# Optimization experiments

Hardware: AMD Instinct MI355X
Metric: run time of the kernel (lower is better)

## Reference

```python
import jax, jax.numpy as jnp
import numpy as np

C = 128   # recurrent/value channels
CK = 64   # key channels

def conv1x1(x, W, b):
    # x: [B,Cin,H,W], W: [Cout,Cin], b: [Cout]
    return jnp.einsum('bchw,oc->bohw', x, W) + b[None, :, None, None]

def extract_windows(x):
    # zero-padded 3x3 windows, matching F.unfold(kernel=3, padding=1)
    # x: [B,C,H2,W2] -> [B,C,9,H2,W2], tap order = (ky, kx) row-major
    B, c, H2, W2 = x.shape
    xp = jnp.pad(x, ((0, 0), (0, 0), (1, 1), (1, 1)))
    taps = [xp[:, :, dy:dy + H2, dx:dx + W2] for dy in range(3) for dx in range(3)]
    return jnp.stack(taps, axis=2)

def setup_inputs() -> dict:
    key = jax.random.key(0)
    ks = jax.random.split(key, 12)
    B, H, W = 2, 256, 512
    H2, W2 = 128, 256
    s = 0.02
    return {
        'h_prev': jax.random.normal(ks[0], (B, C, H2, W2), jnp.float32),
        'h_init': jax.random.normal(ks[1], (B, C, H, W), jnp.float32),
        'Wq':   jax.random.normal(ks[2], (CK, C), jnp.float32) * s,
        'bq':   jnp.zeros((CK,), jnp.float32),
        'Wk':   jax.random.normal(ks[3], (CK, C), jnp.float32) * s,
        'bk':   jnp.zeros((CK,), jnp.float32),
        'Wvp':  jax.random.normal(ks[4], (C, C), jnp.float32) * s,
        'bvp':  jnp.zeros((C,), jnp.float32),
        'Wvi':  jax.random.normal(ks[5], (C, C), jnp.float32) * s,
        'bvi':  jnp.zeros((C,), jnp.float32),
        'Wout': jax.random.normal(ks[6], (C, C), jnp.float32) * s,
        'bout': jnp.zeros((C,), jnp.float32),
    }

def reference(h_prev, h_init, Wq, bq, Wk, bk, Wvp, bvp, Wvi, bvi, Wout, bout):
    B, _, H, W = h_init.shape
    _, _, H2, W2 = h_prev.shape
    ry, rx = H // H2, W // W2

    q = conv1x1(h_init, Wq, bq)        # [B,CK,H,W]
    k = conv1x1(h_prev, Wk, bk)        # [B,CK,H2,W2]
    v = conv1x1(h_prev, Wvp, bvp)      # [B,C,H2,W2]

    k_win = extract_windows(k)         # [B,CK,9,H2,W2]
    v_win = extract_windows(v)         # [B,C,9,H2,W2]

    # q at fine res, grouped by coarse cell (nearest-neighbor broadcast of k/v)
    q_r = q.transpose(0, 2, 3, 1).reshape(B, H2, ry, W2, rx, CK)  # [B,H2,ry,W2,rx,CK]
    # scores over 9 window taps (zero-padded taps give score 0, as in unfold)
    scores = jnp.einsum('byaxdc,bcjyx->byaxdj', q_r, k_win)       # [B,H2,ry,W2,rx,9]
    a = jax.nn.softmax(scores, axis=-1)
    x = jnp.einsum('byaxdj,bcjyx->bcyaxd', a, v_win)              # [B,C,H2,ry,W2,rx]
    x = x.reshape(B, C, H, W)

    v_init = conv1x1(h_init, Wvi, bvi)
    return conv1x1(v_init + x, Wout, bout)
```

## Files before the change

kernel.cpp:

```cpp
#include <hip/hip_runtime.h>
#include <cstdint>
#include <cstddef>

#define THREADS 256
#define FTHREADS 512

typedef __attribute__((ext_vector_type(8))) short short8;
typedef __attribute__((ext_vector_type(4))) float f32x4;

#define MFMA(a, b, c) __builtin_amdgcn_mfma_f32_16x16x32_bf16((a), (b), (c), 0, 0, 0)

static constexpr int kC    = 128;
static constexpr int kImgC = 128 * 256;
static constexpr int kImgF = 256 * 512;

__device__ __forceinline__ unsigned short f2bf(float f) {
  unsigned u = __builtin_bit_cast(unsigned, f);
  u += 0x7fffu + ((u >> 16) & 1u);
  return (unsigned short)(u >> 16);
}
__device__ __forceinline__ unsigned pack_bf16(float lo, float hi) {
  return (unsigned)f2bf(lo) | ((unsigned)f2bf(hi) << 16);
}
__device__ __forceinline__ float bf_up(unsigned short u) {
  return __builtin_bit_cast(float, (unsigned)u << 16);
}
__device__ __forceinline__ float bf_lo(unsigned u) {
  return __builtin_bit_cast(float, u << 16);
}
__device__ __forceinline__ float bf_hi(unsigned u) {
  return __builtin_bit_cast(float, u & 0xffff0000u);
}

__device__ __forceinline__ short8 ldA(const char* lds, int mt, int kt, int l) {
  const int px = mt * 16 + (l & 15);
  const int chunk = (kt * 4 + (l >> 4)) ^ (px & 7);
  return *(const short8*)(lds + px * 256 + chunk * 16);
}

__global__ __launch_bounds__(THREADS) void cast_w(
    const float* __restrict__ Wq, const float* __restrict__ Wk,
    const float* __restrict__ Wvp, const float* __restrict__ Wvi,
    const float* __restrict__ Wout, unsigned short* __restrict__ dst) {
  int i = blockIdx.x * THREADS + threadIdx.x;
  float v;
  if (i < 8192)       v = Wq[i];
  else if (i < 16384) v = Wk[i - 8192];
  else if (i < 32768) v = Wvp[i - 16384];
  else if (i < 49152) v = Wvi[i - 32768];
  else                v = Wout[i - 49152];
  dst[i] = f2bf(v);
}

__global__ __launch_bounds__(THREADS, 4) void coarse_kv(
    const float* __restrict__ h_prev, const unsigned short* __restrict__ wbuf,
    const float* __restrict__ bk, const float* __restrict__ bvp,
    unsigned short* __restrict__ kbuf, unsigned short* __restrict__ vbuf) {
  __shared__ char xs[16384];
  const int tid = threadIdx.x;
  const int l = tid & 63, w = tid >> 6;
  const int m = l & 15, g = l >> 4;
  const int chq = w * 16 + m;

  const int tile = blockIdx.x;
  const int b    = tile >> 9;
  const int p0   = (tile & 511) * 64;
  const int p0g  = tile * 64;

  const short8* wkp = (const short8*)(wbuf + 8192);
  const short8* wvp = (const short8*)(wbuf + 16384);
  short8 fk[4], fv[2][4];
  #pragma unroll
  for (int kt = 0; kt < 4; ++kt) fk[kt] = wkp[chq * 16 + kt * 4 + g];
  #pragma unroll
  for (int nt = 0; nt < 2; ++nt)
    #pragma unroll
    for (int kt = 0; kt < 4; ++kt)
      fv[nt][kt] = wvp[(nt * 64 + chq) * 16 + kt * 4 + g];

  {
    const float* src = h_prev + (size_t)b * kC * kImgC + p0;
    const int pxl = l & 7, cg = l >> 3;
    #pragma unroll
    for (int i = 0; i < 16; ++i) {
      const int px = pxl + 8 * (i & 7);
      const int c  = 2 * (cg + 8 * (w + 4 * (i >> 3)));
      float f0 = src[(size_t)c * kImgC + px];
      float f1 = src[(size_t)(c + 1) * kImgC + px];
      const int chunk = (c >> 3) ^ (px & 7);
      *(unsigned*)(xs + px * 256 + chunk * 16 + (c & 7) * 2) = pack_bf16(f0, f1);
    }
  }
  __syncthreads();

  {
    const float bl = bk[chq];
    #pragma unroll
    for (int mt = 0; mt < 4; ++mt) {
      f32x4 acc = {bl, bl, bl, bl};
      #pragma unroll
      for (int kt = 0; kt < 4; ++kt) acc = MFMA(ldA(xs, mt, kt, l), fk[kt], acc);
      #pragma unroll
      for (int r = 0; r < 4; ++r)
        kbuf[(size_t)(p0g + mt * 16 + g * 4 + r) * 64 + chq] = f2bf(acc[r]);
    }
  }
  #pragma unroll
  for (int nt = 0; nt < 2; ++nt) {
    const float bl = bvp[nt * 64 + chq];
    #pragma unroll
    for (int mt = 0; mt < 4; ++mt) {
      f32x4 acc = {bl, bl, bl, bl};
      #pragma unroll
      for (int kt = 0; kt < 4; ++kt) acc = MFMA(ldA(xs, mt, kt, l), fv[nt][kt], acc);
      #pragma unroll
      for (int r = 0; r < 4; ++r)
        vbuf[(size_t)(p0g + mt * 16 + g * 4 + r) * 128 + nt * 64 + chq] = f2bf(acc[r]);
    }
  }
}

__global__ __launch_bounds__(FTHREADS, 4) void fine_fused(
    const float* __restrict__ h_init, const unsigned short* __restrict__ wbuf,
    const float* __restrict__ bq, const float* __restrict__ bvi,
    const float* __restrict__ bout,
    const unsigned short* __restrict__ kbuf, const unsigned short* __restrict__ vbuf,
    float* __restrict__ out) {
  __shared__ char xs[32768];
  __shared__ unsigned short qs[128 * 72];
  __shared__ unsigned short ks_[60 * 80];
  __shared__ unsigned short vs_[60 * 144];

  const int tid = threadIdx.x;
  const int l = tid & 63, w = tid >> 6;
  const int m = l & 15, g = l >> 4;

  const int bid = blockIdx.x;
  const int b   = bid >> 10;
  const int r10 = bid & 1023;
  const int ty  = r10 >> 5;
  const int tx  = r10 & 31;
  const int y0  = ty * 8;
  const int x0  = tx * 16;
  const int y20 = y0 >> 1;
  const int x20 = x0 >> 1;

  const size_t fbase = (size_t)b * kC * kImgF;
  const unsigned short* kb = kbuf + (size_t)b * kImgC * 64;
  const unsigned short* vb = vbuf + (size_t)b * kImgC * 128;

  const short8* wqp = (const short8*)wbuf;
  const short8* wip = (const short8*)(wbuf + 32768);
  const short8* wop = (const short8*)(wbuf + 49152);

  {
    const int half = tid >> 8;
    const int tl = tid & 255;
    const int sl = tl & 63, sw = tl >> 6;
    const int pxl = sl & 7, cg = sl >> 3;
    #pragma unroll
    for (int i = 0; i < 16; ++i) {
      const int px = half * 64 + pxl + 8 * (i & 7);
      const int row = px >> 4, col = px & 15;
      const int c  = 2 * (cg + 8 * (sw + 4 * (i >> 3)));
      const size_t off = (size_t)(y0 + row) * 512 + x0 + col;
      float f0 = h_init[fbase + (size_t)c * kImgF + off];
      float f1 = h_init[fbase + (size_t)(c + 1) * kImgF + off];
      const int chunk = (c >> 3) ^ (px & 7);
      *(unsigned*)(xs + px * 256 + chunk * 16 + (c & 7) * 2) = pack_bf16(f0, f1);
    }
  }

  #pragma unroll
  for (int it = 0; it < 2; ++it) {
    const int i = tid + it * 512;
    if (i < 960) {
      const int cell = i >> 4, cp = i & 15;
      const int cy = cell / 10, cx = cell - cy * 10;
      const int yy = y20 + cy - 1, xx = x20 + cx - 1;
      uint2 val = make_uint2(0u, 0u);
      if ((unsigned)yy < 128u && (unsigned)xx < 256u)
        val = *(const uint2*)(kb + ((size_t)yy * 256 + xx) * 64 + cp * 4);
      *(uint2*)((char*)ks_ + cell * 160 + (cp >> 2) * 40 + (cp & 3) * 8) = val;
    }
  }
  #pragma unroll
  for (int it = 0; it < 4; ++it) {
    const int i = tid + it * 512;
    if (i < 1920) {
      const int cell = i >> 5, cp = i & 31;
      const int cy = cell / 10, cx = cell - cy * 10;
      const int yy = y20 + cy - 1, xx = x20 + cx - 1;
      uint2 val = make_uint2(0u, 0u);
      if ((unsigned)yy < 128u && (unsigned)xx < 256u)
        val = *(const uint2*)(vb + ((size_t)yy * 256 + xx) * 128 + cp * 4);
      *(uint2*)((char*)vs_ + cell * 288 + (cp >> 3) * 72 + (cp & 7) * 8) = val;
    }
  }
  __syncthreads();

  const int chq4 = (w & 3) * 16 + m;
  const int hh   = w >> 2;
  {
    short8 fq[4];
    #pragma unroll
    for (int kt = 0; kt < 4; ++kt) fq[kt] = wqp[chq4 * 16 + kt * 4 + g];
    const float bl = bq[chq4];
    #pragma unroll
    for (int mt = 0; mt < 4; ++mt) {
      f32x4 acc = {bl, bl, bl, bl};
      #pragma unroll
      for (int kt = 0; kt < 4; ++kt) acc = MFMA(ldA(xs, hh * 4 + mt, kt, l), fq[kt], acc);
      #pragma unroll
      for (int r = 0; r < 4; ++r)
        qs[(hh * 64 + mt * 16 + g * 4 + r) * 72 + chq4] = f2bf(acc[r]);
    }
  }

  const int ch = w * 16 + m;
  f32x4 vacc[8];
  {
    short8 fi[4];
    #pragma unroll
    for (int kt = 0; kt < 4; ++kt) fi[kt] = wip[ch * 16 + kt * 4 + g];
    const float bl = bvi[ch];
    #pragma unroll
    for (int mt = 0; mt < 8; ++mt) {
      f32x4 acc = {bl, bl, bl, bl};
      #pragma unroll
      for (int kt = 0; kt < 4; ++kt) acc = MFMA(ldA(xs, mt, kt, l), fi[kt], acc);
      vacc[mt] = acc;
    }
  }
  __syncthreads();

  #pragma unroll
  for (int mt = 0; mt < 8; ++mt) {
    #pragma unroll
    for (int r = 0; r < 4; ++r) {
      const int px = mt * 16 + g * 4 + r;
      const int chunk = (ch >> 3) ^ (px & 7);
      *(unsigned short*)(xs + px * 256 + chunk * 16 + (ch & 7) * 2) = f2bf(vacc[mt][r]);
    }
  }
  __syncthreads();

  {
    const int apx = tid >> 2;
    const int sub = tid & 3;
    const int r2  = apx >> 5;
    const int c2  = (apx & 15) >> 1;

    float qf[16];
    {
      const uint4* qp = (const uint4*)((const char*)qs + apx * 144 + sub * 32);
      const uint4 u0 = qp[0], u1 = qp[1];
      const unsigned uu[8] = {u0.x, u0.y, u0.z, u0.w, u1.x, u1.y, u1.z, u1.w};
      #pragma unroll
      for (int i = 0; i < 8; ++i) {
        qf[2 * i]     = bf_lo(uu[i]);
        qf[2 * i + 1] = bf_hi(uu[i]);
      }
    }

    float a[9];
    #pragma unroll
    for (int j = 0; j < 9; ++j) {
      const int cell = (r2 + j / 3) * 10 + c2 + (j % 3);
      const char* kc = (const char*)ks_ + cell * 160 + sub * 40;
      const uint2 u0 = *(const uint2*)kc;
      const uint2 u1 = *(const uint2*)(kc + 8);
      const uint2 u2 = *(const uint2*)(kc + 16);
      const uint2 u3 = *(const uint2*)(kc + 24);
      const unsigned uu[8] = {u0.x, u0.y, u1.x, u1.y, u2.x, u2.y, u3.x, u3.y};
      float s = 0.f;
      #pragma unroll
      for (int i = 0; i < 8; ++i)
        s += qf[2 * i] * bf_lo(uu[i]) + qf[2 * i + 1] * bf_hi(uu[i]);
      s += __shfl_xor(s, 1);
      s += __shfl_xor(s, 2);
      a[j] = s;
    }
    float mx = a[0];
    #pragma unroll
    for (int j = 1; j < 9; ++j) mx = fmaxf(mx, a[j]);
    float den = 0.f;
    #pragma unroll
    for (int j = 0; j < 9; ++j) { a[j] = __expf(a[j] - mx); den += a[j]; }
    const float inv = 1.f / den;

    float tt[32];
    #pragma unroll
    for (int i = 0; i < 32; ++i) tt[i] = 0.f;
    #pragma unroll
    for (int j = 0; j < 9; ++j) {
      const int cell = (r2 + j / 3) * 10 + c2 + (j % 3);
      const float aj = a[j] * inv;
      const char* vc = (const char*)vs_ + cell * 288 + sub * 72;
      #pragma unroll
      for (int q2 = 0; q2 < 8; ++q2) {
        const uint2 u = *(const uint2*)(vc + q2 * 8);
        tt[4 * q2]     += aj * bf_lo(u.x);
        tt[4 * q2 + 1] += aj * bf_hi(u.x);
        tt[4 * q2 + 2] += aj * bf_lo(u.y);
        tt[4 * q2 + 3] += aj * bf_hi(u.y);
      }
    }
    #pragma unroll
    for (int i = 0; i < 16; ++i) {
      const int cc2 = sub * 32 + 2 * i;
      const int chunk = (cc2 >> 3) ^ (apx & 7);
      unsigned* p = (unsigned*)(xs + apx * 256 + chunk * 16 + (cc2 & 7) * 2);
      const unsigned u = *p;
      const float lo = bf_lo(u) + tt[2 * i];
      const float hi = bf_up((unsigned short)(u >> 16)) + tt[2 * i + 1];
      *p = pack_bf16(lo, hi);
    }
  }
  __syncthreads();

  {
    short8 fo[4];
    #pragma unroll
    for (int kt = 0; kt < 4; ++kt) fo[kt] = wop[ch * 16 + kt * 4 + g];
    const float bl = bout[ch];
    #pragma unroll
    for (int mt = 0; mt < 8; ++mt) {
      f32x4 acc = {bl, bl, bl, bl};
      #pragma unroll
      for (int kt = 0; kt < 4; ++kt) acc = MFMA(ldA(xs, mt, kt, l), fo[kt], acc);
      *(float4*)(out + fbase + (size_t)ch * kImgF
                 + (size_t)(y0 + mt) * 512 + x0 + g * 4) =
          make_float4(acc[0], acc[1], acc[2], acc[3]);
    }
  }
}

extern "C" void kernel_launch(void* const* d_in, const int* in_sizes, int n_in,
                              void* d_out, int out_size, void* d_ws, size_t ws_size,
                              hipStream_t stream) {
  const float* h_prev = (const float*)d_in[0];
  const float* h_init = (const float*)d_in[1];
  const float* Wq   = (const float*)d_in[2];
  const float* bq   = (const float*)d_in[3];
  const float* Wk   = (const float*)d_in[4];
  const float* bk   = (const float*)d_in[5];
  const float* Wvp  = (const float*)d_in[6];
  const float* bvp  = (const float*)d_in[7];
  const float* Wvi  = (const float*)d_in[8];
  const float* bvi  = (const float*)d_in[9];
  const float* Wout = (const float*)d_in[10];
  const float* bout = (const float*)d_in[11];
  float* out = (float*)d_out;

  char* ws = (char*)d_ws;
  unsigned short* wbuf = (unsigned short*)ws;
  unsigned short* kbuf = (unsigned short*)(ws + 131072);
  unsigned short* vbuf = (unsigned short*)(ws + 131072 + (size_t)65536 * 64 * 2);

  cast_w<<<256, THREADS, 0, stream>>>(Wq, Wk, Wvp, Wvi, Wout, wbuf);
  coarse_kv<<<1024, THREADS, 0, stream>>>(h_prev, wbuf, bk, bvp, kbuf, vbuf);
  fine_fused<<<2048, FTHREADS, 0, stream>>>(h_init, wbuf, bq, bvi, bout,
                                            kbuf, vbuf, out);
}
```

Baseline: 369.0 us.

## Fold Wvi into Wout and vectorize attention FMAs with packed float2

```diff
diff --git a/kernel.cpp b/kernel.cpp
--- a/kernel.cpp
+++ b/kernel.cpp
@@ -7,6 +7,7 @@
 
 typedef __attribute__((ext_vector_type(8))) short short8;
 typedef __attribute__((ext_vector_type(4))) float f32x4;
+typedef __attribute__((ext_vector_type(2))) float f32x2;
 
 #define MFMA(a, b, c) __builtin_amdgcn_mfma_f32_16x16x32_bf16((a), (b), (c), 0, 0, 0)
 
@@ -22,14 +23,14 @@
 __device__ __forceinline__ unsigned pack_bf16(float lo, float hi) {
   return (unsigned)f2bf(lo) | ((unsigned)f2bf(hi) << 16);
 }
-__device__ __forceinline__ float bf_up(unsigned short u) {
-  return __builtin_bit_cast(float, (unsigned)u << 16);
-}
 __device__ __forceinline__ float bf_lo(unsigned u) {
   return __builtin_bit_cast(float, u << 16);
 }
 __device__ __forceinline__ float bf_hi(unsigned u) {
   return __builtin_bit_cast(float, u & 0xffff0000u);
+}
+__device__ __forceinline__ f32x2 bf_up2(unsigned u) {
+  return (f32x2){bf_lo(u), bf_hi(u)};
 }
 
 __device__ __forceinline__ short8 ldA(const char* lds, int mt, int kt, int l) {
@@ -52,6 +53,23 @@
   dst[i] = f2bf(v);
 }
 
+__global__ __launch_bounds__(THREADS) void fuse_w(
+    const float* __restrict__ Wvi, const float* __restrict__ bvi,
+    const float* __restrict__ Wout, const float* __restrict__ bout,
+    unsigned short* __restrict__ wf, float* __restrict__ bf) {
+  const int idx = blockIdx.x * THREADS + threadIdx.x;
+  const int o = idx >> 7, c = idx & 127;
+  float s = 0.f;
+  #pragma unroll 4
+  for (int m2 = 0; m2 < 128; ++m2) s += Wout[o * 128 + m2] * Wvi[m2 * 128 + c];
+  wf[idx] = f2bf(s);
+  if (c == 0) {
+    float sb = bout[o];
+    for (int m2 = 0; m2 < 128; ++m2) sb += Wout[o * 128 + m2] * bvi[m2];
+    bf[o] = sb;
+  }
+}
+
 __global__ __launch_bounds__(THREADS, 4) void coarse_kv(
     const float* __restrict__ h_prev, const unsigned short* __restrict__ wbuf,
     const float* __restrict__ bk, const float* __restrict__ bvp,
@@ -122,8 +140,8 @@
 
 __global__ __launch_bounds__(FTHREADS, 4) void fine_fused(
     const float* __restrict__ h_init, const unsigned short* __restrict__ wbuf,
-    const float* __restrict__ bq, const float* __restrict__ bvi,
-    const float* __restrict__ bout,
+    const unsigned short* __restrict__ wf, const float* __restrict__ bfused,
+    const float* __restrict__ bq,
     const unsigned short* __restrict__ kbuf, const unsigned short* __restrict__ vbuf,
     float* __restrict__ out) {
   __shared__ char xs[32768];
@@ -150,7 +168,7 @@
   const unsigned short* vb = vbuf + (size_t)b * kImgC * 128;
 
   const short8* wqp = (const short8*)wbuf;
-  const short8* wip = (const short8*)(wbuf + 32768);
+  const short8* wfp = (const short8*)wf;
   const short8* wop = (const short8*)(wbuf + 49152);
 
   {
@@ -218,29 +236,18 @@
   }
 
   const int ch = w * 16 + m;
-  f32x4 vacc[8];
-  {
-    short8 fi[4];
-    #pragma unroll
-    for (int kt = 0; kt < 4; ++kt) fi[kt] = wip[ch * 16 + kt * 4 + g];
-    const float bl = bvi[ch];
+  f32x4 accO[8];
+  {
+    short8 ff[4];
+    #pragma unroll
+    for (int kt = 0; kt < 4; ++kt) ff[kt] = wfp[ch * 16 + kt * 4 + g];
+    const float bl = bfused[ch];
     #pragma unroll
     for (int mt = 0; mt < 8; ++mt) {
       f32x4 acc = {bl, bl, bl, bl};
       #pragma unroll
-      for (int kt = 0; kt < 4; ++kt) acc = MFMA(ldA(xs, mt, kt, l), fi[kt], acc);
-      vacc[mt] = acc;
-    }
-  }
-  __syncthreads();
-
-  #pragma unroll
-  for (int mt = 0; mt < 8; ++mt) {
-    #pragma unroll
-    for (int r = 0; r < 4; ++r) {
-      const int px = mt * 16 + g * 4 + r;
-      const int chunk = (ch >> 3) ^ (px & 7);
-      *(unsigned short*)(xs + px * 256 + chunk * 16 + (ch & 7) * 2) = f2bf(vacc[mt][r]);
+      for (int kt = 0; kt < 4; ++kt) acc = MFMA(ldA(xs, mt, kt, l), ff[kt], acc);
+      accO[mt] = acc;
     }
   }
   __syncthreads();
@@ -251,16 +258,13 @@
     const int r2  = apx >> 5;
     const int c2  = (apx & 15) >> 1;
 
-    float qf[16];
+    f32x2 qf2[8];
     {
       const uint4* qp = (const uint4*)((const char*)qs + apx * 144 + sub * 32);
       const uint4 u0 = qp[0], u1 = qp[1];
       const unsigned uu[8] = {u0.x, u0.y, u0.z, u0.w, u1.x, u1.y, u1.z, u1.w};
       #pragma unroll
-      for (int i = 0; i < 8; ++i) {
-        qf[2 * i]     = bf_lo(uu[i]);
-        qf[2 * i + 1] = bf_hi(uu[i]);
-      }
+      for (int i = 0; i < 8; ++i) qf2[i] = bf_up2(uu[i]);
     }
 
     float a[9];
@@ -273,10 +277,11 @@
       const uint2 u2 = *(const uint2*)(kc + 16);
       const uint2 u3 = *(const uint2*)(kc + 24);
       const unsigned uu[8] = {u0.x, u0.y, u1.x, u1.y, u2.x, u2.y, u3.x, u3.y};
-      float s = 0.f;
+      f32x2 s2 = {0.f, 0.f};
       #pragma unroll
       for (int i = 0; i < 8; ++i)
-        s += qf[2 * i] * bf_lo(uu[i]) + qf[2 * i + 1] * bf_hi(uu[i]);
+        s2 = __builtin_elementwise_fma(qf2[i], bf_up2(uu[i]), s2);
+      float s = s2.x + s2.y;
       s += __shfl_xor(s, 1);
       s += __shfl_xor(s, 2);
       a[j] = s;
@@ -289,32 +294,28 @@
     for (int j = 0; j < 9; ++j) { a[j] = __expf(a[j] - mx); den += a[j]; }
     const float inv = 1.f / den;
 
-    float tt[32];
-    #pragma unroll
-    for (int i = 0; i < 32; ++i) tt[i] = 0.f;
+    f32x2 tt2[16];
+    #pragma unroll
+    for (int i = 0; i < 16; ++i) tt2[i] = (f32x2){0.f, 0.f};
     #pragma unroll
     for (int j = 0; j < 9; ++j) {
       const int cell = (r2 + j / 3) * 10 + c2 + (j % 3);
       const float aj = a[j] * inv;
+      const f32x2 aj2 = {aj, aj};
       const char* vc = (const char*)vs_ + cell * 288 + sub * 72;
       #pragma unroll
       for (int q2 = 0; q2 < 8; ++q2) {
         const uint2 u = *(const uint2*)(vc + q2 * 8);
-        tt[4 * q2]     += aj * bf_lo(u.x);
-        tt[4 * q2 + 1] += aj * bf_hi(u.x);
-        tt[4 * q2 + 2] += aj * bf_lo(u.y);
-        tt[4 * q2 + 3] += aj * bf_hi(u.y);
+        tt2[2 * q2]     = __builtin_elementwise_fma(bf_up2(u.x), aj2, tt2[2 * q2]);
+        tt2[2 * q2 + 1] = __builtin_elementwise_fma(bf_up2(u.y), aj2, tt2[2 * q2 + 1]);
       }
     }
     #pragma unroll
     for (int i = 0; i < 16; ++i) {
       const int cc2 = sub * 32 + 2 * i;
       const int chunk = (cc2 >> 3) ^ (apx & 7);
-      unsigned* p = (unsigned*)(xs + apx * 256 + chunk * 16 + (cc2 & 7) * 2);
-      const unsigned u = *p;
-      const float lo = bf_lo(u) + tt[2 * i];
-      const float hi = bf_up((unsigned short)(u >> 16)) + tt[2 * i + 1];
-      *p = pack_bf16(lo, hi);
+      *(unsigned*)(xs + apx * 256 + chunk * 16 + (cc2 & 7) * 2) =
+          pack_bf16(tt2[i].x, tt2[i].y);
     }
   }
   __syncthreads();
@@ -323,10 +324,9 @@
     short8 fo[4];
     #pragma unroll
     for (int kt = 0; kt < 4; ++kt) fo[kt] = wop[ch * 16 + kt * 4 + g];
-    const float bl = bout[ch];
     #pragma unroll
     for (int mt = 0; mt < 8; ++mt) {
-      f32x4 acc = {bl, bl, bl, bl};
+      f32x4 acc = accO[mt];
       #pragma unroll
       for (int kt = 0; kt < 4; ++kt) acc = MFMA(ldA(xs, mt, kt, l), fo[kt], acc);
       *(float4*)(out + fbase + (size_t)ch * kImgF
@@ -355,11 +355,14 @@
 
   char* ws = (char*)d_ws;
   unsigned short* wbuf = (unsigned short*)ws;
-  unsigned short* kbuf = (unsigned short*)(ws + 131072);
-  unsigned short* vbuf = (unsigned short*)(ws + 131072 + (size_t)65536 * 64 * 2);
+  unsigned short* wfb  = (unsigned short*)(ws + 131072);
+  float* bfb           = (float*)(ws + 164352 - 512);
+  unsigned short* kbuf = (unsigned short*)(ws + 164352);
+  unsigned short* vbuf = (unsigned short*)(ws + 164352 + (size_t)8388608);
 
   cast_w<<<256, THREADS, 0, stream>>>(Wq, Wk, Wvp, Wvi, Wout, wbuf);
+  fuse_w<<<64, THREADS, 0, stream>>>(Wvi, bvi, Wout, bout, wfb, bfb);
   coarse_kv<<<1024, THREADS, 0, stream>>>(h_prev, wbuf, bk, bvp, kbuf, vbuf);
-  fine_fused<<<2048, FTHREADS, 0, stream>>>(h_init, wbuf, bq, bvi, bout,
+  fine_fused<<<2048, FTHREADS, 0, stream>>>(h_init, wbuf, wfb, bfb, bq,
                                             kbuf, vbuf, out);
 }
```

Result: slower. 383.3 us (+3.9%).
